# Kernel tuning notes

Hardware: AMD Instinct MI355X
Metric: run time of the kernel (lower is better)

## Reference

```python
import jax, jax.numpy as jnp
import numpy as np

B, L = 8, 2048
AMP, ANG = 48, 16
H = 4
AQK, GQK = 12, 6   # amp/ang qk head dims
AV, GV = 12, 6     # amp/ang v head dims
LOOKBACK = 100


def setup_inputs() -> dict:
    key = jax.random.key(0)
    ks = jax.random.split(key, 16)
    def w(k, i, o):
        # kaiming-uniform-ish scale; stored [in, out] so forward is x @ W
        bound = 1.0 / np.sqrt(i)
        return jax.random.uniform(k, (i, o), jnp.float32, -bound, bound)
    return dict(
        x_ang=jax.random.normal(ks[0], (B, L, 2 * ANG), jnp.float32),
        x_amp=jax.random.normal(ks[1], (B, L, AMP), jnp.float32),
        Wq_amp=w(ks[2], AMP, H * AQK),
        Wk_amp=w(ks[3], AMP, H * AQK),
        Wv_amp=w(ks[4], AMP, H * AV),
        Wq_ang_r=w(ks[5], ANG, H * GQK),
        Wq_ang_i=w(ks[6], ANG, H * GQK),
        Wk_ang_r=w(ks[7], ANG, H * GQK),
        Wk_ang_i=w(ks[8], ANG, H * GQK),
        Wv_ang_r=w(ks[9], ANG, H * GV),
        Wv_ang_i=w(ks[10], ANG, H * GV),
        Wout_amp=w(ks[11], H * AV, AMP),
        bout_amp=jax.random.uniform(ks[12], (AMP,), jnp.float32, -0.1, 0.1),
        Wout_ang_r=w(ks[13], H * GV, ANG),
        Wout_ang_i=w(ks[14], H * GV, ANG),
    )


def _clin(xr, xi, Wr, Wi):
    # complex linear: (xr + i xi) @ (Wr + i Wi)
    return xr @ Wr - xi @ Wi, xr @ Wi + xi @ Wr


def reference(x_ang, x_amp, Wq_amp, Wk_amp, Wv_amp,
              Wq_ang_r, Wq_ang_i, Wk_ang_r, Wk_ang_i,
              Wv_ang_r, Wv_ang_i, Wout_amp, bout_amp,
              Wout_ang_r, Wout_ang_i):
    Bb, Ll, CA = x_ang.shape
    ang_r, ang_i = jnp.split(x_ang, 2, axis=-1)

    def heads(x, hd):  # [B,L,H*hd] -> [B,H,L,hd]
        return x.reshape(Bb, Ll, H, hd).transpose(0, 2, 1, 3)

    q_amp = heads(x_amp @ Wq_amp, AQK)
    k_amp = heads(x_amp @ Wk_amp, AQK)
    qar, qai = _clin(ang_r, ang_i, Wq_ang_r, Wq_ang_i)
    kar, kai = _clin(ang_r, ang_i, Wk_ang_r, Wk_ang_i)
    q = jnp.concatenate([heads(qar, GQK), heads(qai, GQK), q_amp], axis=-1)  # [B,H,L,24]
    k = jnp.concatenate([heads(kar, GQK), heads(kai, GQK), k_amp], axis=-1)

    v_amp = heads(x_amp @ Wv_amp, AV)
    var, vai = _clin(ang_r, ang_i, Wv_ang_r, Wv_ang_i)
    v = jnp.concatenate([heads(var, GV), heads(vai, GV), v_amp], axis=-1)  # [B,H,L,24]

    scale = 1.0 / jnp.sqrt(jnp.asarray(q.shape[-1], q.dtype))
    scores = jnp.einsum('bhqd,bhkd->bhqk', q, k) * scale
    idx = jnp.arange(Ll)
    valid = (idx[None, :] <= idx[:, None]) & (idx[None, :] >= idx[:, None] - (LOOKBACK - 1))
    mask = jnp.where(valid, jnp.asarray(0.0, scores.dtype), jnp.finfo(scores.dtype).min)
    attn = jax.nn.softmax(scores + mask, axis=-1)
    out = jnp.einsum('bhqk,bhkd->bhqd', attn, v)  # [B,H,L,24]

    o_ang_r, o_ang_i, o_amp = jnp.split(out, [GV, 2 * GV], axis=-1)

    def merge(x):  # [B,H,L,hd] -> [B,L,H*hd]
        return x.transpose(0, 2, 1, 3).reshape(Bb, Ll, -1)

    out_amp = merge(o_amp) @ Wout_amp + bout_amp
    out_ang_r, out_ang_i = _clin(merge(o_ang_r), merge(o_ang_i), Wout_ang_r, Wout_ang_i)
    return (out_ang_r, out_ang_i, out_amp)
```

## Files before the change

kernel.cpp:

```cpp
#include <hip/hip_runtime.h>
#include <hip/hip_bf16.h>

constexpr int B = 8;
constexpr int L = 2048;
constexpr int ANG = 16;
constexpr int AMP = 48;
constexpr int H = 4;
constexpr int AQK = 12, GQK = 6;
constexpr int AV = 12, GV = 6;
constexpr int HD = 2 * GQK + AQK;
constexpr int LOOKBACK = 100;
constexpr int NTOK = B * L;

constexpr int TQ     = 64;
constexpr int GROUPS = 4;
constexpr int MAXK   = TQ + LOOKBACK - 1;
constexpr int NT     = L / TQ;

struct StageT {
    float xam[MAXK][49];
    float xan[MAXK][33];
};
struct TileT {
    float4 Ks[MAXK][8];
    float4 Vs[MAXK][8];
    float4 Qs[TQ][6];
};
union SharedU { StageT stage; TileT t; };

__global__ __launch_bounds__(256) void fused_qkv_attn_kernel(
    const float* __restrict__ x_ang, const float* __restrict__ x_amp,
    const float* __restrict__ Wq_amp, const float* __restrict__ Wk_amp,
    const float* __restrict__ Wv_amp,
    const float* __restrict__ Wq_ang_r, const float* __restrict__ Wq_ang_i,
    const float* __restrict__ Wk_ang_r, const float* __restrict__ Wk_ang_i,
    const float* __restrict__ Wv_ang_r, const float* __restrict__ Wv_ang_i,
    float* __restrict__ att)
{
    __shared__ SharedU u;
    __shared__ float  Pm[GROUPS][TQ];
    __shared__ float  Ps[GROUPS][TQ];
    __shared__ float4 Po[GROUPS][TQ][6];

    const int tid = threadIdx.x;
    const int bh  = blockIdx.x / NT;
    const int qt  = blockIdx.x % NT;
    const int b   = bh / H, h = bh % H;
    const int q0  = qt * TQ;
    int kmin = q0 - (LOOKBACK - 1); if (kmin < 0) kmin = 0;
    const int nrows = (q0 + TQ - 1) - kmin + 1;
    const int qoff  = q0 - kmin;

    {
        const float4* xm4 = (const float4*)(x_amp + ((size_t)b * L + kmin) * AMP);
        const float4* xg4 = (const float4*)(x_ang + ((size_t)b * L + kmin) * (2 * ANG));
        int namp = nrows * 12;
        int ntot = namp + nrows * 8;
        for (int c = tid; c < ntot; c += 256) {
            if (c < namp) {
                int r = c / 12, i = c % 12;
                float4 t = xm4[c];
                float* p = &u.stage.xam[r][4 * i];
                p[0] = t.x; p[1] = t.y; p[2] = t.z; p[3] = t.w;
            } else {
                int c2 = c - namp;
                int r = c2 / 8, i = c2 % 8;
                float4 t = xg4[c2];
                float* p = &u.stage.xan[r][4 * i];
                p[0] = t.x; p[1] = t.y; p[2] = t.z; p[3] = t.w;
            }
        }
    }
    __syncthreads();

    float4 kout[6], vout[6], qout[6];
    const bool kvact = (tid < nrows);
    const bool qact  = (tid >= 192);
    const int  qrow  = tid - 192;

    #pragma unroll
    for (int s = 0; s < 6; ++s) {
        if (kvact) {
            int r = tid;
            if (s >= 3) {
                int col4 = h * AQK + (s - 3) * 4;
                const float* Wk = Wk_amp + col4;
                const float* Wv = Wv_amp + col4;
                float4 ka = {0,0,0,0}, va = {0,0,0,0};
                #pragma unroll
                for (int i = 0; i < AMP; ++i) {
                    float x = u.stage.xam[r][i];
                    float4 wk = *(const float4*)(Wk + i * 48);
                    float4 wv = *(const float4*)(Wv + i * 48);
                    ka.x += x * wk.x; ka.y += x * wk.y; ka.z += x * wk.z; ka.w += x * wk.w;
                    va.x += x * wv.x; va.y += x * wv.y; va.z += x * wv.z; va.w += x * wv.w;
                }
                kout[s] = ka; vout[s] = va;
            } else {
                float kk[4], vv[4];
                #pragma unroll
                for (int c = 0; c < 4; ++c) {
                    int d = 4 * s + c;
                    bool re = (d < GQK);
                    int dd = re ? d : d - GQK;
                    int col = h * GQK + dd;
                    const float* WkA = re ? Wk_ang_r : Wk_ang_i;
                    const float* WkB = re ? Wk_ang_i : Wk_ang_r;
                    const float* WvA = re ? Wv_ang_r : Wv_ang_i;
                    const float* WvB = re ? Wv_ang_i : Wv_ang_r;
                    float sgn = re ? -1.f : 1.f;
                    float ak = 0, bk = 0, aw = 0, bw = 0;
                    #pragma unroll
                    for (int i = 0; i < ANG; ++i) {
                        float xr = u.stage.xan[r][i];
                        float xi = u.stage.xan[r][16 + i];
                        ak += xr * WkA[i * 24 + col];  bk += xi * WkB[i * 24 + col];
                        aw += xr * WvA[i * 24 + col];  bw += xi * WvB[i * 24 + col];
                    }
                    kk[c] = ak + sgn * bk;  vv[c] = aw + sgn * bw;
                }
                kout[s] = make_float4(kk[0], kk[1], kk[2], kk[3]);
                vout[s] = make_float4(vv[0], vv[1], vv[2], vv[3]);
            }
        }
        if (qact) {
            int r = qoff + qrow;
            if (s >= 3) {
                int col4 = h * AQK + (s - 3) * 4;
                const float* Wq = Wq_amp + col4;
                float4 qa = {0,0,0,0};
                #pragma unroll
                for (int i = 0; i < AMP; ++i) {
                    float x = u.stage.xam[r][i];
                    float4 wq = *(const float4*)(Wq + i * 48);
                    qa.x += x * wq.x; qa.y += x * wq.y; qa.z += x * wq.z; qa.w += x * wq.w;
                }
                qout[s] = qa;
            } else {
                float qq[4];
                #pragma unroll
                for (int c = 0; c < 4; ++c) {
                    int d = 4 * s + c;
                    bool re = (d < GQK);
                    int dd = re ? d : d - GQK;
                    int col = h * GQK + dd;
                    const float* WA = re ? Wq_ang_r : Wq_ang_i;
                    const float* WB = re ? Wq_ang_i : Wq_ang_r;
                    float sgn = re ? -1.f : 1.f;
                    float aa = 0, bb = 0;
                    #pragma unroll
                    for (int i = 0; i < ANG; ++i) {
                        float xr = u.stage.xan[r][i];
                        float xi = u.stage.xan[r][16 + i];
                        aa += xr * WA[i * 24 + col];  bb += xi * WB[i * 24 + col];
                    }
                    qq[c] = aa + sgn * bb;
                }
                qout[s] = make_float4(qq[0], qq[1], qq[2], qq[3]);
            }
        }
    }
    __syncthreads();

    if (kvact) {
        int r = tid, rx = r & 7;
        #pragma unroll
        for (int s = 0; s < 6; ++s) {
            u.t.Ks[r][s ^ rx] = kout[s];
            u.t.Vs[r][s ^ rx] = vout[s];
        }
    }
    if (qact) {
        #pragma unroll
        for (int s = 0; s < 6; ++s) u.t.Qs[qrow][s] = qout[s];
    }
    __syncthreads();

    const int qlocal = tid & (TQ - 1);
    const int group  = tid >> 6;
    const int qi = q0 + qlocal;

    float4 qr4[6];
    #pragma unroll
    for (int s = 0; s < 6; ++s) qr4[s] = u.t.Qs[qlocal][s];

    const float scale = 0.2041241452319315f;
    float m = -3.0e38f, ss = 0.f;
    float4 o4[6];
    #pragma unroll
    for (int s = 0; s < 6; ++s) { o4[s].x = 0.f; o4[s].y = 0.f; o4[s].z = 0.f; o4[s].w = 0.f; }

    int j0 = qi - (LOOKBACK - 1); if (j0 < 0) j0 = 0;
    for (int j = j0 + group; j <= qi; j += GROUPS) {
        int r  = j - kmin;
        int rx = r & 7;
        float sc = 0.f;
        #pragma unroll
        for (int s = 0; s < 6; ++s) {
            float4 kk = u.t.Ks[r][s ^ rx];
            sc += qr4[s].x * kk.x + qr4[s].y * kk.y + qr4[s].z * kk.z + qr4[s].w * kk.w;
        }
        sc *= scale;
        float mn   = fmaxf(m, sc);
        float corr = __expf(m - mn);
        float p    = __expf(sc - mn);
        ss = ss * corr + p;
        #pragma unroll
        for (int s = 0; s < 6; ++s) {
            float4 vv = u.t.Vs[r][s ^ rx];
            o4[s].x = o4[s].x * corr + p * vv.x;
            o4[s].y = o4[s].y * corr + p * vv.y;
            o4[s].z = o4[s].z * corr + p * vv.z;
            o4[s].w = o4[s].w * corr + p * vv.w;
        }
        m = mn;
    }

    Pm[group][qlocal] = m;
    Ps[group][qlocal] = ss;
    #pragma unroll
    for (int s = 0; s < 6; ++s) Po[group][qlocal][s] = o4[s];
    __syncthreads();

    {
        int qq    = tid & 63;
        int chunk = tid >> 6;
        float m0 = Pm[0][qq], m1 = Pm[1][qq], m2 = Pm[2][qq], m3 = Pm[3][qq];
        float mm = fmaxf(fmaxf(m0, m1), fmaxf(m2, m3));
        float c0 = __expf(m0 - mm), c1 = __expf(m1 - mm);
        float c2 = __expf(m2 - mm), c3 = __expf(m3 - mm);
        float denom = Ps[0][qq] * c0 + Ps[1][qq] * c1 + Ps[2][qq] * c2 + Ps[3][qq] * c3;
        float inv = 1.f / denom;

        float4* op4 = (float4*)att + (size_t)(b * L + q0 + qq) * 6 * H / H * H;
        op4 = (float4*)att + ((size_t)(b * L + q0 + qq) * H + h) * 0;
        float4* dst = (float4*)att + (size_t)(b * L + q0 + qq) * 24 + h * 6;

        int s = chunk;
        {
            float4 a0 = Po[0][qq][s], a1 = Po[1][qq][s], a2 = Po[2][qq][s], a3 = Po[3][qq][s];
            float4 acc;
            acc.x = (a0.x * c0 + a1.x * c1 + a2.x * c2 + a3.x * c3) * inv;
            acc.y = (a0.y * c0 + a1.y * c1 + a2.y * c2 + a3.y * c3) * inv;
            acc.z = (a0.z * c0 + a1.z * c1 + a2.z * c2 + a3.z * c3) * inv;
            acc.w = (a0.w * c0 + a1.w * c1 + a2.w * c2 + a3.w * c3) * inv;
            dst[s] = acc;
        }
        if (chunk < 2) {
            s = chunk + 4;
            float4 a0 = Po[0][qq][s], a1 = Po[1][qq][s], a2 = Po[2][qq][s], a3 = Po[3][qq][s];
            float4 acc;
            acc.x = (a0.x * c0 + a1.x * c1 + a2.x * c2 + a3.x * c3) * inv;
            acc.y = (a0.y * c0 + a1.y * c1 + a2.y * c2 + a3.y * c3) * inv;
            acc.z = (a0.z * c0 + a1.z * c1 + a2.z * c2 + a3.z * c3) * inv;
            acc.w = (a0.w * c0 + a1.w * c1 + a2.w * c2 + a3.w * c3) * inv;
            dst[s] = acc;
        }
    }
}

constexpr int PAMP_BLOCKS = (NTOK * 48) / 256;
constexpr int PANG_BLOCKS = (NTOK * 16) / 256;

__global__ __launch_bounds__(256) void proj3_kernel(
    const float* __restrict__ att,
    const float* __restrict__ Wout_amp, const float* __restrict__ bout_amp,
    const float* __restrict__ Wout_ang_r, const float* __restrict__ Wout_ang_i,
    float* __restrict__ out)
{
    constexpr size_t ANG_OUT = (size_t)NTOK * ANG;
    int bid = blockIdx.x;

    if (bid < PAMP_BLOCKS) {
        int g   = bid * 256 + threadIdx.x;
        int col = g % 48;
        int tok = g / 48;
        const float4* at4 = (const float4*)att + (size_t)tok * 24;

        float a[48];
        #pragma unroll
        for (int h = 0; h < H; h++) {
            #pragma unroll
            for (int i = 0; i < 3; i++) {
                float4 t = at4[h * 6 + 3 + i];
                a[h*12 + 4*i+0] = t.x; a[h*12 + 4*i+1] = t.y;
                a[h*12 + 4*i+2] = t.z; a[h*12 + 4*i+3] = t.w;
            }
        }
        float acc = bout_amp[col];
        #pragma unroll
        for (int i = 0; i < 48; i++)
            acc += a[i] * Wout_amp[i * AMP + col];
        out[2 * ANG_OUT + (size_t)tok * AMP + col] = acc;
    } else {
        int g   = (bid - PAMP_BLOCKS) * 256 + threadIdx.x;
        int col = g % 16;
        int tok = g / 16;
        const float4* at4 = (const float4*)att + (size_t)tok * 24;

        float ar[24], ai[24];
        #pragma unroll
        for (int h = 0; h < H; h++) {
            float4 t0 = at4[h*6+0], t1 = at4[h*6+1], t2 = at4[h*6+2];
            ar[h*6+0] = t0.x; ar[h*6+1] = t0.y; ar[h*6+2] = t0.z; ar[h*6+3] = t0.w;
            ar[h*6+4] = t1.x; ar[h*6+5] = t1.y;
            ai[h*6+0] = t1.z; ai[h*6+1] = t1.w;
            ai[h*6+2] = t2.x; ai[h*6+3] = t2.y; ai[h*6+4] = t2.z; ai[h*6+5] = t2.w;
        }
        float accr = 0.f, acci = 0.f;
        #pragma unroll
        for (int i = 0; i < 24; i++) {
            float wr = Wout_ang_r[i * ANG + col], wi = Wout_ang_i[i * ANG + col];
            accr += ar[i] * wr - ai[i] * wi;
            acci += ar[i] * wi + ai[i] * wr;
        }
        out[(size_t)tok * ANG + col]           = accr;
        out[ANG_OUT + (size_t)tok * ANG + col] = acci;
    }
}

extern "C" void kernel_launch(void* const* d_in, const int* in_sizes, int n_in,
                              void* d_out, int out_size, void* d_ws, size_t ws_size,
                              hipStream_t stream)
{
    const float* x_ang      = (const float*)d_in[0];
    const float* x_amp      = (const float*)d_in[1];
    const float* Wq_amp     = (const float*)d_in[2];
    const float* Wk_amp     = (const float*)d_in[3];
    const float* Wv_amp     = (const float*)d_in[4];
    const float* Wq_ang_r   = (const float*)d_in[5];
    const float* Wq_ang_i   = (const float*)d_in[6];
    const float* Wk_ang_r   = (const float*)d_in[7];
    const float* Wk_ang_i   = (const float*)d_in[8];
    const float* Wv_ang_r   = (const float*)d_in[9];
    const float* Wv_ang_i   = (const float*)d_in[10];
    const float* Wout_amp   = (const float*)d_in[11];
    const float* bout_amp   = (const float*)d_in[12];
    const float* Wout_ang_r = (const float*)d_in[13];
    const float* Wout_ang_i = (const float*)d_in[14];

    float* out = (float*)d_out;
    float* att = (float*)d_ws;

    fused_qkv_attn_kernel<<<B * H * NT, 256, 0, stream>>>(
        x_ang, x_amp, Wq_amp, Wk_amp, Wv_amp,
        Wq_ang_r, Wq_ang_i, Wk_ang_r, Wk_ang_i, Wv_ang_r, Wv_ang_i,
        att);

    proj3_kernel<<<PAMP_BLOCKS + PANG_BLOCKS, 256, 0, stream>>>(
        att, Wout_amp, bout_amp, Wout_ang_r, Wout_ang_i, out);
}
```

Before: 153.2 us.

## Use chunked two-pass softmax with shuffle merge and vectorize output projection

```diff
diff --git a/kernel.cpp b/kernel.cpp
--- a/kernel.cpp
+++ b/kernel.cpp
@@ -14,6 +14,7 @@
 
 constexpr int TQ     = 64;
 constexpr int GROUPS = 4;
+constexpr int CHUNK  = 25;
 constexpr int MAXK   = TQ + LOOKBACK - 1;
 constexpr int NT     = L / TQ;
 
@@ -24,11 +25,11 @@
 struct TileT {
     float4 Ks[MAXK][8];
     float4 Vs[MAXK][8];
-    float4 Qs[TQ][6];
+    float4 Qs[TQ][7];
 };
 union SharedU { StageT stage; TileT t; };
 
-__global__ __launch_bounds__(256) void fused_qkv_attn_kernel(
+__global__ __launch_bounds__(256, 3) void fused_qkv_attn3_kernel(
     const float* __restrict__ x_ang, const float* __restrict__ x_amp,
     const float* __restrict__ Wq_amp, const float* __restrict__ Wk_amp,
     const float* __restrict__ Wv_amp,
@@ -38,9 +39,6 @@
     float* __restrict__ att)
 {
     __shared__ SharedU u;
-    __shared__ float  Pm[GROUPS][TQ];
-    __shared__ float  Ps[GROUPS][TQ];
-    __shared__ float4 Po[GROUPS][TQ][6];
 
     const int tid = threadIdx.x;
     const int bh  = blockIdx.x / NT;
@@ -48,7 +46,7 @@
     const int b   = bh / H, h = bh % H;
     const int q0  = qt * TQ;
     int kmin = q0 - (LOOKBACK - 1); if (kmin < 0) kmin = 0;
-    const int nrows = (q0 + TQ - 1) - kmin + 1;
+    const int nrows = q0 + TQ - kmin;
     const int qoff  = q0 - kmin;
 
     {
@@ -73,7 +71,7 @@
     }
     __syncthreads();
 
-    float4 kout[6], vout[6], qout[6];
+    float4 kpack[6], vpack[6], qpack[6];
     const bool kvact = (tid < nrows);
     const bool qact  = (tid >= 192);
     const int  qrow  = tid - 192;
@@ -95,7 +93,7 @@
                     ka.x += x * wk.x; ka.y += x * wk.y; ka.z += x * wk.z; ka.w += x * wk.w;
                     va.x += x * wv.x; va.y += x * wv.y; va.z += x * wv.z; va.w += x * wv.w;
                 }
-                kout[s] = ka; vout[s] = va;
+                kpack[s] = ka; vpack[s] = va;
             } else {
                 float kk[4], vv[4];
                 #pragma unroll
@@ -119,8 +117,8 @@
                     }
                     kk[c] = ak + sgn * bk;  vv[c] = aw + sgn * bw;
                 }
-                kout[s] = make_float4(kk[0], kk[1], kk[2], kk[3]);
-                vout[s] = make_float4(vv[0], vv[1], vv[2], vv[3]);
+                kpack[s] = make_float4(kk[0], kk[1], kk[2], kk[3]);
+                vpack[s] = make_float4(vv[0], vv[1], vv[2], vv[3]);
             }
         }
         if (qact) {
@@ -135,7 +133,7 @@
                     float4 wq = *(const float4*)(Wq + i * 48);
                     qa.x += x * wq.x; qa.y += x * wq.y; qa.z += x * wq.z; qa.w += x * wq.w;
                 }
-                qout[s] = qa;
+                qpack[s] = qa;
             } else {
                 float qq[4];
                 #pragma unroll
@@ -156,7 +154,7 @@
                     }
                     qq[c] = aa + sgn * bb;
                 }
-                qout[s] = make_float4(qq[0], qq[1], qq[2], qq[3]);
+                qpack[s] = make_float4(qq[0], qq[1], qq[2], qq[3]);
             }
         }
     }
@@ -166,103 +164,116 @@
         int r = tid, rx = r & 7;
         #pragma unroll
         for (int s = 0; s < 6; ++s) {
-            u.t.Ks[r][s ^ rx] = kout[s];
-            u.t.Vs[r][s ^ rx] = vout[s];
-        }
+            u.t.Ks[r][s ^ rx] = kpack[s];
+            u.t.Vs[r][s ^ rx] = vpack[s];
+        }
+    } else if (tid < MAXK) {
+        float4 z = make_float4(0.f,0.f,0.f,0.f);
+        #pragma unroll
+        for (int s = 0; s < 6; ++s) { u.t.Ks[tid][s] = z; u.t.Vs[tid][s] = z; }
     }
     if (qact) {
         #pragma unroll
-        for (int s = 0; s < 6; ++s) u.t.Qs[qrow][s] = qout[s];
+        for (int s = 0; s < 6; ++s) u.t.Qs[qrow][s] = qpack[s];
     }
     __syncthreads();
 
-    const int qlocal = tid & (TQ - 1);
-    const int group  = tid >> 6;
-    const int qi = q0 + qlocal;
-
-    float4 qr4[6];
-    #pragma unroll
-    for (int s = 0; s < 6; ++s) qr4[s] = u.t.Qs[qlocal][s];
+    const int lane = tid & 63;
+    const int w    = tid >> 6;
+    const int q16  = lane & 15;
+    const int g    = lane >> 4;
+    const int ql   = w * 16 + q16;
+    const int qi   = q0 + ql;
+
+    float4 q4[6];
+    #pragma unroll
+    for (int s = 0; s < 6; ++s) q4[s] = u.t.Qs[ql][s];
 
     const float scale = 0.2041241452319315f;
-    float m = -3.0e38f, ss = 0.f;
-    float4 o4[6];
-    #pragma unroll
-    for (int s = 0; s < 6; ++s) { o4[s].x = 0.f; o4[s].y = 0.f; o4[s].z = 0.f; o4[s].w = 0.f; }
-
     int j0 = qi - (LOOKBACK - 1); if (j0 < 0) j0 = 0;
-    for (int j = j0 + group; j <= qi; j += GROUPS) {
+    const int jstart = j0 + g;
+
+    float sc[CHUNK];
+    #pragma unroll
+    for (int t = 0; t < CHUNK; ++t) {
+        int j  = jstart + t * GROUPS;
         int r  = j - kmin;
         int rx = r & 7;
-        float sc = 0.f;
+        float d = 0.f;
         #pragma unroll
         for (int s = 0; s < 6; ++s) {
             float4 kk = u.t.Ks[r][s ^ rx];
-            sc += qr4[s].x * kk.x + qr4[s].y * kk.y + qr4[s].z * kk.z + qr4[s].w * kk.w;
-        }
-        sc *= scale;
-        float mn   = fmaxf(m, sc);
-        float corr = __expf(m - mn);
-        float p    = __expf(sc - mn);
-        ss = ss * corr + p;
+            d += q4[s].x*kk.x + q4[s].y*kk.y + q4[s].z*kk.z + q4[s].w*kk.w;
+        }
+        sc[t] = (j <= qi) ? d * scale : -3.0e38f;
+    }
+    float m = sc[0];
+    #pragma unroll
+    for (int t = 1; t < CHUNK; ++t) m = fmaxf(m, sc[t]);
+    float ssum = 0.f;
+    #pragma unroll
+    for (int t = 0; t < CHUNK; ++t) {
+        float p = __expf(sc[t] - m);
+        p = (sc[t] > -1.0e37f) ? p : 0.f;
+        sc[t] = p;
+        ssum += p;
+    }
+    float4 o[6];
+    #pragma unroll
+    for (int s = 0; s < 6; ++s) o[s] = make_float4(0.f,0.f,0.f,0.f);
+    #pragma unroll
+    for (int t = 0; t < CHUNK; ++t) {
+        float p  = sc[t];
+        int j    = jstart + t * GROUPS;
+        int r    = j - kmin;
+        int rx   = r & 7;
         #pragma unroll
         for (int s = 0; s < 6; ++s) {
             float4 vv = u.t.Vs[r][s ^ rx];
-            o4[s].x = o4[s].x * corr + p * vv.x;
-            o4[s].y = o4[s].y * corr + p * vv.y;
-            o4[s].z = o4[s].z * corr + p * vv.z;
-            o4[s].w = o4[s].w * corr + p * vv.w;
-        }
-        m = mn;
-    }
-
-    Pm[group][qlocal] = m;
-    Ps[group][qlocal] = ss;
-    #pragma unroll
-    for (int s = 0; s < 6; ++s) Po[group][qlocal][s] = o4[s];
-    __syncthreads();
+            o[s].x += p * vv.x; o[s].y += p * vv.y;
+            o[s].z += p * vv.z; o[s].w += p * vv.w;
+        }
+    }
+
+    #pragma unroll
+    for (int d = 16; d <= 32; d <<= 1) {
+        float m2 = __shfl_xor(m, d);
+        float s2 = __shfl_xor(ssum, d);
+        float mm = fmaxf(m, m2);
+        float c1 = __expf(m - mm);
+        float c2 = __expf(m2 - mm);
+        ssum = ssum * c1 + s2 * c2;
+        #pragma unroll
+        for (int s = 0; s < 6; ++s) {
+            o[s].x = o[s].x * c1 + __shfl_xor(o[s].x, d) * c2;
+            o[s].y = o[s].y * c1 + __shfl_xor(o[s].y, d) * c2;
+            o[s].z = o[s].z * c1 + __shfl_xor(o[s].z, d) * c2;
+            o[s].w = o[s].w * c1 + __shfl_xor(o[s].w, d) * c2;
+        }
+        m = mm;
+    }
+    float inv = 1.f / ssum;
 
     {
-        int qq    = tid & 63;
-        int chunk = tid >> 6;
-        float m0 = Pm[0][qq], m1 = Pm[1][qq], m2 = Pm[2][qq], m3 = Pm[3][qq];
-        float mm = fmaxf(fmaxf(m0, m1), fmaxf(m2, m3));
-        float c0 = __expf(m0 - mm), c1 = __expf(m1 - mm);
-        float c2 = __expf(m2 - mm), c3 = __expf(m3 - mm);
-        float denom = Ps[0][qq] * c0 + Ps[1][qq] * c1 + Ps[2][qq] * c2 + Ps[3][qq] * c3;
-        float inv = 1.f / denom;
-
-        float4* op4 = (float4*)att + (size_t)(b * L + q0 + qq) * 6 * H / H * H;
-        op4 = (float4*)att + ((size_t)(b * L + q0 + qq) * H + h) * 0;
-        float4* dst = (float4*)att + (size_t)(b * L + q0 + qq) * 24 + h * 6;
-
-        int s = chunk;
-        {
-            float4 a0 = Po[0][qq][s], a1 = Po[1][qq][s], a2 = Po[2][qq][s], a3 = Po[3][qq][s];
-            float4 acc;
-            acc.x = (a0.x * c0 + a1.x * c1 + a2.x * c2 + a3.x * c3) * inv;
-            acc.y = (a0.y * c0 + a1.y * c1 + a2.y * c2 + a3.y * c3) * inv;
-            acc.z = (a0.z * c0 + a1.z * c1 + a2.z * c2 + a3.z * c3) * inv;
-            acc.w = (a0.w * c0 + a1.w * c1 + a2.w * c2 + a3.w * c3) * inv;
-            dst[s] = acc;
-        }
-        if (chunk < 2) {
-            s = chunk + 4;
-            float4 a0 = Po[0][qq][s], a1 = Po[1][qq][s], a2 = Po[2][qq][s], a3 = Po[3][qq][s];
-            float4 acc;
-            acc.x = (a0.x * c0 + a1.x * c1 + a2.x * c2 + a3.x * c3) * inv;
-            acc.y = (a0.y * c0 + a1.y * c1 + a2.y * c2 + a3.y * c3) * inv;
-            acc.z = (a0.z * c0 + a1.z * c1 + a2.z * c2 + a3.z * c3) * inv;
-            acc.w = (a0.w * c0 + a1.w * c1 + a2.w * c2 + a3.w * c3) * inv;
-            dst[s] = acc;
+        float4* dst = (float4*)att + (size_t)(b * L + qi) * 24 + h * 6;
+        if (g == 0) {
+            dst[0] = make_float4(o[0].x*inv, o[0].y*inv, o[0].z*inv, o[0].w*inv);
+            dst[4] = make_float4(o[4].x*inv, o[4].y*inv, o[4].z*inv, o[4].w*inv);
+        } else if (g == 1) {
+            dst[1] = make_float4(o[1].x*inv, o[1].y*inv, o[1].z*inv, o[1].w*inv);
+            dst[5] = make_float4(o[5].x*inv, o[5].y*inv, o[5].z*inv, o[5].w*inv);
+        } else if (g == 2) {
+            dst[2] = make_float4(o[2].x*inv, o[2].y*inv, o[2].z*inv, o[2].w*inv);
+        } else {
+            dst[3] = make_float4(o[3].x*inv, o[3].y*inv, o[3].z*inv, o[3].w*inv);
         }
     }
 }
 
-constexpr int PAMP_BLOCKS = (NTOK * 48) / 256;
-constexpr int PANG_BLOCKS = (NTOK * 16) / 256;
-
-__global__ __launch_bounds__(256) void proj3_kernel(
+constexpr int PJ_AMP_BLOCKS = (NTOK * 12) / 256;
+constexpr int PJ_ANG_BLOCKS = (NTOK * 4) / 256;
+
+__global__ __launch_bounds__(256) void proj4_kernel(
     const float* __restrict__ att,
     const float* __restrict__ Wout_amp, const float* __restrict__ bout_amp,
     const float* __restrict__ Wout_ang_r, const float* __restrict__ Wout_ang_i,
@@ -271,51 +282,58 @@
     constexpr size_t ANG_OUT = (size_t)NTOK * ANG;
     int bid = blockIdx.x;
 
-    if (bid < PAMP_BLOCKS) {
-        int g   = bid * 256 + threadIdx.x;
-        int col = g % 48;
-        int tok = g / 48;
+    if (bid < PJ_AMP_BLOCKS) {
+        int gidx = bid * 256 + threadIdx.x;
+        int c4   = (gidx % 12) * 4;
+        int tok  = gidx / 12;
         const float4* at4 = (const float4*)att + (size_t)tok * 24;
 
         float a[48];
         #pragma unroll
-        for (int h = 0; h < H; h++) {
+        for (int h = 0; h < H; ++h) {
             #pragma unroll
-            for (int i = 0; i < 3; i++) {
+            for (int i = 0; i < 3; ++i) {
                 float4 t = at4[h * 6 + 3 + i];
-                a[h*12 + 4*i+0] = t.x; a[h*12 + 4*i+1] = t.y;
-                a[h*12 + 4*i+2] = t.z; a[h*12 + 4*i+3] = t.w;
+                a[h*12 + 4*i+0]=t.x; a[h*12 + 4*i+1]=t.y;
+                a[h*12 + 4*i+2]=t.z; a[h*12 + 4*i+3]=t.w;
             }
         }
-        float acc = bout_amp[col];
-        #pragma unroll
-        for (int i = 0; i < 48; i++)
-            acc += a[i] * Wout_amp[i * AMP + col];
-        out[2 * ANG_OUT + (size_t)tok * AMP + col] = acc;
+        float4 acc = *(const float4*)(bout_amp + c4);
+        #pragma unroll
+        for (int i = 0; i < 48; ++i) {
+            float4 w = *(const float4*)(Wout_amp + i * 48 + c4);
+            acc.x += a[i]*w.x; acc.y += a[i]*w.y; acc.z += a[i]*w.z; acc.w += a[i]*w.w;
+        }
+        *(float4*)(out + 2*ANG_OUT + (size_t)tok * 48 + c4) = acc;
     } else {
-        int g   = (bid - PAMP_BLOCKS) * 256 + threadIdx.x;
-        int col = g % 16;
-        int tok = g / 16;
+        int gidx = (bid - PJ_AMP_BLOCKS) * 256 + threadIdx.x;
+        int c4   = (gidx % 4) * 4;
+        int tok  = gidx / 4;
         const float4* at4 = (const float4*)att + (size_t)tok * 24;
 
         float ar[24], ai[24];
         #pragma unroll
-        for (int h = 0; h < H; h++) {
+        for (int h = 0; h < H; ++h) {
             float4 t0 = at4[h*6+0], t1 = at4[h*6+1], t2 = at4[h*6+2];
-            ar[h*6+0] = t0.x; ar[h*6+1] = t0.y; ar[h*6+2] = t0.z; ar[h*6+3] = t0.w;
-            ar[h*6+4] = t1.x; ar[h*6+5] = t1.y;
-            ai[h*6+0] = t1.z; ai[h*6+1] = t1.w;
-            ai[h*6+2] = t2.x; ai[h*6+3] = t2.y; ai[h*6+4] = t2.z; ai[h*6+5] = t2.w;
-        }
-        float accr = 0.f, acci = 0.f;
-        #pragma unroll
-        for (int i = 0; i < 24; i++) {
-            float wr = Wout_ang_r[i * ANG + col], wi = Wout_ang_i[i * ANG + col];
-            accr += ar[i] * wr - ai[i] * wi;
-            acci += ar[i] * wi + ai[i] * wr;
-        }
-        out[(size_t)tok * ANG + col]           = accr;
-        out[ANG_OUT + (size_t)tok * ANG + col] = acci;
+            ar[h*6+0]=t0.x; ar[h*6+1]=t0.y; ar[h*6+2]=t0.z; ar[h*6+3]=t0.w;
+            ar[h*6+4]=t1.x; ar[h*6+5]=t1.y;
+            ai[h*6+0]=t1.z; ai[h*6+1]=t1.w;
+            ai[h*6+2]=t2.x; ai[h*6+3]=t2.y; ai[h*6+4]=t2.z; ai[h*6+5]=t2.w;
+        }
+        float4 accr = make_float4(0.f,0.f,0.f,0.f);
+        float4 acci = make_float4(0.f,0.f,0.f,0.f);
+        #pragma unroll
+        for (int i = 0; i < 24; ++i) {
+            float4 wr = *(const float4*)(Wout_ang_r + i * 16 + c4);
+            float4 wi = *(const float4*)(Wout_ang_i + i * 16 + c4);
+            float r = ar[i], im = ai[i];
+            accr.x += r*wr.x - im*wi.x;  accr.y += r*wr.y - im*wi.y;
+            accr.z += r*wr.z - im*wi.z;  accr.w += r*wr.w - im*wi.w;
+            acci.x += r*wi.x + im*wr.x;  acci.y += r*wi.y + im*wr.y;
+            acci.z += r*wi.z + im*wr.z;  acci.w += r*wi.w + im*wr.w;
+        }
+        *(float4*)(out + (size_t)tok * 16 + c4)           = accr;
+        *(float4*)(out + ANG_OUT + (size_t)tok * 16 + c4) = acci;
     }
 }
 
@@ -342,11 +360,11 @@
     float* out = (float*)d_out;
     float* att = (float*)d_ws;
 
-    fused_qkv_attn_kernel<<<B * H * NT, 256, 0, stream>>>(
+    fused_qkv_attn3_kernel<<<B * H * NT, 256, 0, stream>>>(
         x_ang, x_amp, Wq_amp, Wk_amp, Wv_amp,
         Wq_ang_r, Wq_ang_i, Wk_ang_r, Wk_ang_i, Wv_ang_r, Wv_ang_i,
         att);
 
-    proj3_kernel<<<PAMP_BLOCKS + PANG_BLOCKS, 256, 0, stream>>>(
+    proj4_kernel<<<PJ_AMP_BLOCKS + PJ_ANG_BLOCKS, 256, 0, stream>>>(
         att, Wout_amp, bout_amp, Wout_ang_r, Wout_ang_i, out);
 }
```

Result: faster. 149.5 us (-2.4%).
